# Performance work log

Hardware: AMD Instinct MI355X
Metric: run time of the kernel (lower is better)

## Reference

```python
import jax, jax.numpy as jnp
import numpy as np

NUM_KNOWN_CLASSES = 19  # matches init_kwargs; labels include one extra 'void' class index 19
EPS = 1e-12  # torch F.normalize eps


def setup_inputs() -> dict:
    key = jax.random.key(0)
    k1, k2 = jax.random.split(key)
    features = jax.random.normal(k1, (16, 256, 128, 128), dtype=jnp.float32)
    labels = jax.random.randint(k2, (16, 128, 128), 0, NUM_KNOWN_CLASSES + 1, dtype=jnp.int64)
    return {"features": features, "labels": labels}


def reference(features, labels):
    bs, feat_len, h, w = features.shape
    # L2-normalize each pixel's feature vector over the channel dim (torch F.normalize, p=2, dim=1)
    norm = jnp.maximum(jnp.linalg.norm(features, axis=1, keepdims=True), EPS)
    feats = features / norm
    # [bs, F, h, w] -> [bs*h*w, F]
    feats = jnp.transpose(feats, (0, 2, 3, 1)).reshape(bs * h * w, feat_len)
    labs = labels.reshape(bs * h * w)
    # per-class scatter-sum (equivalent to features.T @ one_hot(labels)), shape [C+1, F]
    protos = jax.ops.segment_sum(feats, labs, num_segments=NUM_KNOWN_CLASSES + 1)
    # drop void class, transpose to [F, C]
    protos = protos[:-1].T
    # L2-normalize each prototype column (dim=0)
    pnorm = jnp.maximum(jnp.linalg.norm(protos, axis=0, keepdims=True), EPS)
    return protos / pnorm
```

## Files before the change

kernel.cpp:

```cpp
#include <hip/hip_runtime.h>
#include <math.h>

#define NCLS 19
#define NF   256
#define HW   16384
#define ROWW 128
#define PAD  257
#define C2   (HW/2)

__global__ __launch_bounds__(256) void zero_protos(float* __restrict__ g) {
    int i = blockIdx.x * 256 + threadIdx.x;
    if (i < NCLS * NF) g[i] = 0.f;
}

__global__ __launch_bounds__(256) void accum_protos(const float* __restrict__ feat,
                                                    const int* __restrict__ labels,
                                                    float* __restrict__ gproto) {
    __shared__ float lds[NCLS * PAD];
    for (int i = threadIdx.x; i < NCLS * PAD; i += 256) lds[i] = 0.f;
    __syncthreads();

    const int tid = threadIdx.x;
    const int r   = tid >> 6;
    const int w0  = (tid & 63) * 2;
    const int row = blockIdx.x * 4 + r;
    const int b   = row >> 7;
    const int h   = row & 127;

    const int2 lab = *(const int2*)(labels + row * ROWW + w0);
    const bool a0 = (lab.x < NCLS);
    const bool a1 = (lab.y < NCLS);

    if (a0 | a1) {
        const float2* p = (const float2*)(feat + ((size_t)b * NF * HW + (size_t)h * ROWW + w0));

        float s0 = 0.f, s1 = 0.f;
        for (int f = 0; f < NF; f += 16) {
            float2 v[16];
            #pragma unroll
            for (int u = 0; u < 16; ++u) v[u] = p[(f + u) * C2];
            #pragma unroll
            for (int u = 0; u < 16; ++u) {
                s0 += v[u].x * v[u].x;
                s1 += v[u].y * v[u].y;
            }
        }
        const float r0 = a0 ? (1.f / fmaxf(sqrtf(s0), 1e-12f)) : 0.f;
        const float r1 = a1 ? (1.f / fmaxf(sqrtf(s1), 1e-12f)) : 0.f;
        const int  o0 = lab.x * PAD;
        const int  o1 = lab.y * PAD;

        for (int f = 0; f < NF; f += 8) {
            float2 v[8];
            #pragma unroll
            for (int u = 0; u < 8; ++u) v[u] = p[(f + u) * C2];
            #pragma unroll
            for (int u = 0; u < 8; ++u) {
                if (a0) atomicAdd(&lds[o0 + f + u], v[u].x * r0);
                if (a1) atomicAdd(&lds[o1 + f + u], v[u].y * r1);
            }
        }
    }
    __syncthreads();

    for (int i = threadIdx.x; i < NCLS * NF; i += 256) {
        const int c = i >> 8;
        const int f = i & 255;
        const float v = lds[c * PAD + (i & 255)];
        if (v != 0.f) atomicAdd(&gproto[(c << 8) | (i & 255)], v);
    }
}

__global__ __launch_bounds__(256) void normalize_protos(const float* __restrict__ gproto,
                                                        float* __restrict__ out) {
    __shared__ float ws[4];
    const int c = blockIdx.x;
    const int f = threadIdx.x;
    const float v = gproto[c * NF + f];

    float s = v * v;
    #pragma unroll
    for (int off = 32; off > 0; off >>= 1) s += __shfl_down(s, off, 64);
    if ((f & 63) == 0) ws[f >> 6] = s;
    __syncthreads();
    const float tot = ws[0] + ws[1] + ws[2] + ws[3];
    const float rn = 1.f / fmaxf(sqrtf(tot), 1e-12f);
    out[f * NCLS + c] = v * rn;
}

extern "C" void kernel_launch(void* const* d_in, const int* in_sizes, int n_in,
                              void* d_out, int out_size, void* d_ws, size_t ws_size,
                              hipStream_t stream) {
    const float* feat   = (const float*)d_in[0];
    const int*   labels = (const int*)d_in[1];
    float* out    = (float*)d_out;
    float* gproto = (float*)d_ws;

    zero_protos<<<NCLS, 256, 0, stream>>>(gproto);
    accum_protos<<<512, 256, 0, stream>>>(feat, labels, gproto);
    normalize_protos<<<NCLS, 256, 0, stream>>>(gproto, out);
}
```

Baseline: 795.2 us.

## Split normalization into sumsq/rinv passes and channel-sliced scatter with float4 loads

Replaces the single row-based accumulation kernel with separate passes. The first computes per-pixel squared norms over channel slices using float4 coalesced loads and global atomics, the second turns them into inverse norms, and the third scatters normalized features for an 8-channel slice into a tiny shared-memory histogram. The aim is better memory coalescing and parallelism, plus a much smaller shared-memory footprint per block. In exchange it adds millions of global atomics on the norm buffer, extra kernel launches, and higher contention on the small per-class shared bins.

Result: faster. 772.8 us (-2.8%).

```diff
diff --git a/kernel.cpp b/kernel.cpp
--- a/kernel.cpp
+++ b/kernel.cpp
@@ -4,70 +4,95 @@
 #define NCLS 19
 #define NF   256
 #define HW   16384
-#define ROWW 128
-#define PAD  257
-#define C2   (HW/2)
+#define NB   16
+#define PX   (NB*HW)
 
-__global__ __launch_bounds__(256) void zero_protos(float* __restrict__ g) {
+__global__ __launch_bounds__(256) void zero_ws(float* __restrict__ nrm2,
+                                               float* __restrict__ gproto) {
     int i = blockIdx.x * 256 + threadIdx.x;
-    if (i < NCLS * NF) g[i] = 0.f;
+    if (i < PX) nrm2[i] = 0.f;
+    if (i < NCLS * NF) gproto[i] = 0.f;
 }
 
-__global__ __launch_bounds__(256) void accum_protos(const float* __restrict__ feat,
-                                                    const int* __restrict__ labels,
-                                                    float* __restrict__ gproto) {
-    __shared__ float lds[NCLS * PAD];
-    for (int i = threadIdx.x; i < NCLS * PAD; i += 256) lds[i] = 0.f;
+__global__ __launch_bounds__(256) void sumsq_kernel(const float* __restrict__ feat,
+                                                    float* __restrict__ nrm2) {
+    const int g  = blockIdx.x;
+    const int b  = g >> 5;
+    const int f0 = (g & 31) << 3;
+    const int t  = threadIdx.x;
+
+    const float* base = feat + (size_t)(b * NF + f0) * HW + t * 4;
+    float* np = nrm2 + b * HW + t * 4;
+
+    for (int k = 0; k < 16; ++k) {
+        float4 v[8];
+        #pragma unroll
+        for (int s = 0; s < 8; ++s)
+            v[s] = *(const float4*)(base + (size_t)s * HW + k * 1024);
+        float a0 = 0.f, a1 = 0.f, a2 = 0.f, a3 = 0.f;
+        #pragma unroll
+        for (int s = 0; s < 8; ++s) {
+            a0 += v[s].x * v[s].x;
+            a1 += v[s].y * v[s].y;
+            a2 += v[s].z * v[s].z;
+            a3 += v[s].w * v[s].w;
+        }
+        atomicAdd(&np[k * 1024 + 0], a0);
+        atomicAdd(&np[k * 1024 + 1], a1);
+        atomicAdd(&np[k * 1024 + 2], a2);
+        atomicAdd(&np[k * 1024 + 3], a3);
+    }
+}
+
+__global__ __launch_bounds__(256) void rinv_kernel(float* __restrict__ nrm2) {
+    int i = (blockIdx.x * 256 + threadIdx.x) * 4;
+    float4 s = *(float4*)(nrm2 + i);
+    float4 r;
+    r.x = 1.f / fmaxf(sqrtf(s.x), 1e-12f);
+    r.y = 1.f / fmaxf(sqrtf(s.y), 1e-12f);
+    r.z = 1.f / fmaxf(sqrtf(s.z), 1e-12f);
+    r.w = 1.f / fmaxf(sqrtf(s.w), 1e-12f);
+    *(float4*)(nrm2 + i) = r;
+}
+
+__global__ __launch_bounds__(256) void scatter_kernel(const float* __restrict__ feat,
+                                                      const int* __restrict__ labels,
+                                                      const float* __restrict__ rinv,
+                                                      float* __restrict__ gproto) {
+    __shared__ float lp[NCLS * 9];
+    const int t = threadIdx.x;
+    for (int i = t; i < NCLS * 9; i += 256) lp[i] = 0.f;
     __syncthreads();
 
-    const int tid = threadIdx.x;
-    const int r   = tid >> 6;
-    const int w0  = (tid & 63) * 2;
-    const int row = blockIdx.x * 4 + r;
-    const int b   = row >> 7;
-    const int h   = row & 127;
+    const int g  = blockIdx.x;
+    const int b  = g >> 5;
+    const int f0 = (g & 31) << 3;
 
-    const int2 lab = *(const int2*)(labels + row * ROWW + w0);
-    const bool a0 = (lab.x < NCLS);
-    const bool a1 = (lab.y < NCLS);
+    const float* base = feat + (size_t)(b * NF + f0) * HW + t * 4;
+    const int*   lb   = labels + b * HW + t * 4;
+    const float* rv   = rinv   + b * HW + t * 4;
 
-    if (a0 | a1) {
-        const float2* p = (const float2*)(feat + ((size_t)b * NF * HW + (size_t)h * ROWW + w0));
-
-        float s0 = 0.f, s1 = 0.f;
-        for (int f = 0; f < NF; f += 16) {
-            float2 v[16];
-            #pragma unroll
-            for (int u = 0; u < 16; ++u) v[u] = p[(f + u) * C2];
-            #pragma unroll
-            for (int u = 0; u < 16; ++u) {
-                s0 += v[u].x * v[u].x;
-                s1 += v[u].y * v[u].y;
-            }
-        }
-        const float r0 = a0 ? (1.f / fmaxf(sqrtf(s0), 1e-12f)) : 0.f;
-        const float r1 = a1 ? (1.f / fmaxf(sqrtf(s1), 1e-12f)) : 0.f;
-        const int  o0 = lab.x * PAD;
-        const int  o1 = lab.y * PAD;
-
-        for (int f = 0; f < NF; f += 8) {
-            float2 v[8];
-            #pragma unroll
-            for (int u = 0; u < 8; ++u) v[u] = p[(f + u) * C2];
-            #pragma unroll
-            for (int u = 0; u < 8; ++u) {
-                if (a0) atomicAdd(&lds[o0 + f + u], v[u].x * r0);
-                if (a1) atomicAdd(&lds[o1 + f + u], v[u].y * r1);
-            }
+    for (int k = 0; k < 16; ++k) {
+        const int4   l4 = *(const int4*)(lb + k * 1024);
+        const float4 r4 = *(const float4*)(rv + k * 1024);
+        float4 v[8];
+        #pragma unroll
+        for (int s = 0; s < 8; ++s)
+            v[s] = *(const float4*)(base + (size_t)s * HW + k * 1024);
+        #pragma unroll
+        for (int s = 0; s < 8; ++s) {
+            if (l4.x < NCLS) atomicAdd(&lp[l4.x * 9 + s], v[s].x * r4.x);
+            if (l4.y < NCLS) atomicAdd(&lp[l4.y * 9 + s], v[s].y * r4.y);
+            if (l4.z < NCLS) atomicAdd(&lp[l4.z * 9 + s], v[s].z * r4.z);
+            if (l4.w < NCLS) atomicAdd(&lp[l4.w * 9 + s], v[s].w * r4.w);
         }
     }
     __syncthreads();
 
-    for (int i = threadIdx.x; i < NCLS * NF; i += 256) {
-        const int c = i >> 8;
-        const int f = i & 255;
-        const float v = lds[c * PAD + (i & 255)];
-        if (v != 0.f) atomicAdd(&gproto[(c << 8) | (i & 255)], v);
+    for (int i = t; i < NCLS * 8; i += 256) {
+        const int c = i >> 3, fr = i & 7;
+        const float val = lp[c * 9 + fr];
+        if (val != 0.f) atomicAdd(&gproto[c * NF + f0 + fr], val);
     }
 }
 
@@ -95,8 +120,11 @@
     const int*   labels = (const int*)d_in[1];
     float* out    = (float*)d_out;
     float* gproto = (float*)d_ws;
+    float* nrm2   = (float*)d_ws + 8192;
 
-    zero_protos<<<NCLS, 256, 0, stream>>>(gproto);
-    accum_protos<<<512, 256, 0, stream>>>(feat, labels, gproto);
+    zero_ws<<<PX / 256, 256, 0, stream>>>(nrm2, gproto);
+    sumsq_kernel<<<512, 256, 0, stream>>>(feat, nrm2);
+    rinv_kernel<<<PX / 1024, 256, 0, stream>>>(nrm2);
+    scatter_kernel<<<512, 256, 0, stream>>>(feat, labels, nrm2, gproto);
     normalize_protos<<<NCLS, 256, 0, stream>>>(gproto, out);
 }
```
